# Optimization experiments

Measured on AMD Instinct MI355X. Metric: run time of the kernel, lower is better.

## Reference

```python
import jax, jax.numpy as jnp
import numpy as np
import math

T, R, H, DK = 3, 4, 8, 32   # num_types, num_relations, n_heads, d_k
OUT = H * DK                # out_dim = 256
IN = 256                    # in_dim (== out_dim, required by residual)
B, N = 4, 1024              # batch, max_nodes
LN_EPS = 1e-5


def setup_inputs() -> dict:
    key = jax.random.key(0)
    ks = jax.random.split(key, 12)
    a = math.sqrt(6.0 / (2 * DK))  # xavier_uniform bound for [d_k,d_k]
    w = 0.02
    return {
        "node_features":   jax.random.normal(ks[0], (B, N, IN), jnp.float32),
        "node_types_soft": jax.random.uniform(ks[1], (B, N, T), jnp.float32),
        "adj_matrix_soft": jax.random.uniform(ks[2], (B, N, N), jnp.float32),
        "edge_types_soft": jax.random.uniform(ks[3], (B, N, N, R), jnp.float32),
        "Wq": jax.random.normal(ks[4], (T, IN, OUT), jnp.float32) * w,
        "bq": jnp.zeros((T, OUT), jnp.float32),
        "Wk": jax.random.normal(ks[5], (T, IN, OUT), jnp.float32) * w,
        "bk": jnp.zeros((T, OUT), jnp.float32),
        "Wv": jax.random.normal(ks[6], (T, IN, OUT), jnp.float32) * w,
        "bv": jnp.zeros((T, OUT), jnp.float32),
        "Wa": jax.random.normal(ks[7], (T, OUT, OUT), jnp.float32) * w,
        "ba": jnp.zeros((T, OUT), jnp.float32),
        "rel_pri": jnp.ones((R, H), jnp.float32),
        "rel_att": jax.random.uniform(ks[8], (R, H, DK, DK), jnp.float32, -a, a),
        "rel_msg": jax.random.uniform(ks[9], (R, H, DK, DK), jnp.float32, -a, a),
        "skip": jnp.ones((T,), jnp.float32),
        "ln_gamma": jnp.ones((T, OUT), jnp.float32),
        "ln_beta": jnp.zeros((T, OUT), jnp.float32),
    }


def _single(x, types, adj, erel, Wq, bq, Wk, bk, Wv, bv, Wa, ba,
            rel_pri, rel_att, rel_msg, skip, ln_gamma, ln_beta):
    # x:[N,in], types:[N,T], adj:[N,N], erel:[N,N,R]
    n = x.shape[0]
    sqrt_dk = float(np.sqrt(DK))
    # per-type projections -> [T,N,H,DK]
    Qt = (jnp.einsum('nd,tdo->tno', x, Wq) + bq[:, None, :]).reshape(T, n, H, DK)
    Kt = (jnp.einsum('nd,tdo->tno', x, Wk) + bk[:, None, :]).reshape(T, n, H, DK)
    Vt = (jnp.einsum('nd,tdo->tno', x, Wv) + bv[:, None, :]).reshape(T, n, H, DK)
    # relation-transformed K/V: [T,R,N,H,DK]
    Ksr = jnp.einsum('tnhd,rhde->trnhe', Kt, rel_att)
    Vsr = jnp.einsum('tnhd,rhde->trnhe', Vt, rel_msg)
    # soft-type mixtures (sums over target/source types factor out of the mask)
    Qbar = jnp.einsum('nt,tnhd->nhd', types, Qt)            # target mix
    Kbar = jnp.einsum('nt,trnhd->rnhd', types, Ksr)         # source mix, per relation
    # accumulated (masked, unnormalized) attention logits [N,N,H]
    res_att = jnp.zeros((n, n, H), x.dtype)
    for r in range(R):
        coef = (adj * erel[:, :, r])[:, :, None] * (rel_pri[r] / sqrt_dk)  # [N,N,H]
        res_att = res_att + coef * jnp.einsum('ihd,jhd->ijh', Qbar, Kbar[r])
    # per-target-row softmax over sources (dim j), zeroed if row-sum tiny
    row_sum = res_att.sum(axis=(1, 2))                       # [N]
    attn = jnp.where((row_sum > 1e-6)[:, None, None],
                     jax.nn.softmax(res_att, axis=1), 0.0)
    # aggregated = sum_{s,r,j} attn * masked score * V_{s,r}  (never builds [N,N,H,DK])
    agg = jnp.zeros((n, H, DK), x.dtype)
    for r in range(R):
        coef = (adj * erel[:, :, r])[:, :, None] * (rel_pri[r] / sqrt_dk)
        for s in range(T):
            score = coef * types[None, :, s, None] * jnp.einsum('ihd,jhd->ijh', Qbar, Ksr[s, r])
            agg = agg + jnp.einsum('ijh,ijh,jhd->ihd', attn, score, Vsr[s, r])
    agg = agg.reshape(n, OUT)
    # per-type output head: a_linear(gelu(agg)), gated residual, layernorm, soft-type mix
    g = jax.nn.gelu(agg, approximate=False)
    trans = jnp.einsum('no,tod->tnd', g, Wa) + ba[:, None, :]          # [T,N,OUT]
    alpha = jax.nn.sigmoid(skip)[:, None, None]
    res = trans * alpha + x[None] * (1.0 - alpha)
    mu = res.mean(axis=-1, keepdims=True)
    var = ((res - mu) ** 2).mean(axis=-1, keepdims=True)
    ln = (res - mu) / jnp.sqrt(var + LN_EPS) * ln_gamma[:, None, :] + ln_beta[:, None, :]
    return jnp.einsum('nt,tnd->nd', types, ln)


def reference(node_features, node_types_soft, adj_matrix_soft, edge_types_soft,
              Wq, bq, Wk, bk, Wv, bv, Wa, ba, rel_pri, rel_att, rel_msg,
              skip, ln_gamma, ln_beta):
    f = jax.vmap(_single, in_axes=(0, 0, 0, 0) + (None,) * 14)
    return f(node_features, node_types_soft, adj_matrix_soft, edge_types_soft,
             Wq, bq, Wk, bk, Wv, bv, Wa, ba, rel_pri, rel_att, rel_msg,
             skip, ln_gamma, ln_beta)
```

## Files before the change

kernel.cpp:

```cpp
#include <hip/hip_runtime.h>
#include <math.h>

constexpr int CB = 4, CN = 1024, CT = 3, CR = 4, CH = 8, CDK = 32, COUT = 256;

typedef __attribute__((ext_vector_type(4))) float f32x4;
typedef __attribute__((ext_vector_type(8))) short s16x8;
typedef __attribute__((ext_vector_type(4))) _Float16 f16x4;
typedef __attribute__((ext_vector_type(8))) _Float16 f16x8;
typedef __attribute__((ext_vector_type(4))) unsigned short u16x4;
typedef __attribute__((ext_vector_type(8))) unsigned short u16x8;

__device__ inline unsigned short f2bf(float x) {
    unsigned u = __float_as_uint(x);
    unsigned r = (u + 0x7fffu + ((u >> 16) & 1u)) >> 16;
    return (unsigned short)r;
}
__device__ inline float bf2f(unsigned short b) {
    return __uint_as_float(((unsigned)b) << 16);
}

__global__ void zero_rs(float* __restrict__ rs) {
    rs[blockIdx.x * 256 + threadIdx.x] = 0.f;
}

__global__ __launch_bounds__(256) void gemm_kernel(
    int mode,
    const float* __restrict__ X,
    const float* __restrict__ W0, const float* __restrict__ W1, const float* __restrict__ W2,
    const float* __restrict__ b0, const float* __restrict__ b1, const float* __restrict__ b2,
    float* __restrict__ Y0, float* __restrict__ Y1, float* __restrict__ Y2)
{
    int z = blockIdx.z;
    int b, t, w3;
    if (mode == 0) { b = z / 9; int r9 = z % 9; w3 = r9 / 3; t = r9 % 3; }
    else           { b = z / CT; t = z % CT; w3 = 0; }
    const float* Xb = X + (size_t)b * CN * COUT;
    const float* W  = (w3 == 0 ? W0 : (w3 == 1 ? W1 : W2)) + (size_t)t * COUT * COUT;
    const float* bs = (w3 == 0 ? b0 : (w3 == 1 ? b1 : b2)) + t * COUT;
    float* Y = (w3 == 0 ? Y0 : (w3 == 1 ? Y1 : Y2)) + ((size_t)b * CT + t) * CN * COUT;

    int row0 = blockIdx.x * 64, col0 = blockIdx.y * 64;
    __shared__ float As[16][65];
    __shared__ float Bsh[16][64];
    int tid = threadIdx.x;
    int tx = tid & 15, ty = tid >> 4;
    float acc[4][4] = {};

    for (int kt = 0; kt < COUT; kt += 16) {
        {
            int m = tid >> 2, k4 = (tid & 3) * 4;
            float4 xv = *(const float4*)(Xb + (size_t)(row0 + m) * COUT + kt + k4);
            As[k4 + 0][m] = xv.x; As[k4 + 1][m] = xv.y;
            As[k4 + 2][m] = xv.z; As[k4 + 3][m] = xv.w;
            int kk = tid >> 4, n4 = (tid & 15) * 4;
            *(float4*)(&Bsh[kk][n4]) = *(const float4*)(W + (size_t)(kt + kk) * COUT + col0 + n4);
        }
        __syncthreads();
        #pragma unroll
        for (int kk = 0; kk < 16; ++kk) {
            float a0 = As[kk][ty * 4 + 0], a1 = As[kk][ty * 4 + 1];
            float a2 = As[kk][ty * 4 + 2], a3 = As[kk][ty * 4 + 3];
            float4 bv = *(const float4*)(&Bsh[kk][tx * 4]);
            acc[0][0] += a0 * bv.x; acc[0][1] += a0 * bv.y; acc[0][2] += a0 * bv.z; acc[0][3] += a0 * bv.w;
            acc[1][0] += a1 * bv.x; acc[1][1] += a1 * bv.y; acc[1][2] += a1 * bv.z; acc[1][3] += a1 * bv.w;
            acc[2][0] += a2 * bv.x; acc[2][1] += a2 * bv.y; acc[2][2] += a2 * bv.z; acc[2][3] += a2 * bv.w;
            acc[3][0] += a3 * bv.x; acc[3][1] += a3 * bv.y; acc[3][2] += a3 * bv.z; acc[3][3] += a3 * bv.w;
        }
        __syncthreads();
    }
    float4 bb = *(const float4*)(bs + col0 + tx * 4);
    #pragma unroll
    for (int im = 0; im < 4; ++im) {
        float4 o;
        o.x = acc[im][0] + bb.x; o.y = acc[im][1] + bb.y;
        o.z = acc[im][2] + bb.z; o.w = acc[im][3] + bb.w;
        *(float4*)(Y + (size_t)(row0 + ty * 4 + im) * COUT + col0 + tx * 4) = o;
    }
}

__global__ void mix_qbar(const float* __restrict__ Qt, const float* __restrict__ types,
                         float* __restrict__ Qbar)
{
    int idx = blockIdx.x * 256 + threadIdx.x;
    int bi = idx >> 6;
    int o4 = (idx & 63) * 4;
    int b = bi >> 10;
    const float* tp = types + (size_t)bi * CT;
    float t0 = tp[0], t1 = tp[1], t2 = tp[2];
    size_t nbase = ((size_t)b * CT) * CN * COUT + (size_t)(bi & 1023) * COUT + o4;
    float4 q0 = *(const float4*)(Qt + nbase);
    float4 q1 = *(const float4*)(Qt + nbase + (size_t)CN * COUT);
    float4 q2 = *(const float4*)(Qt + nbase + 2 * (size_t)CN * COUT);
    float4 o;
    o.x = t0 * q0.x + t1 * q1.x + t2 * q2.x;
    o.y = t0 * q0.y + t1 * q1.y + t2 * q2.y;
    o.z = t0 * q0.z + t1 * q1.z + t2 * q2.z;
    o.w = t0 * q0.w + t1 * q1.w + t2 * q2.w;
    *(float4*)(Qbar + (size_t)bi * COUT + o4) = o;
}

__global__ __launch_bounds__(256) void qr3_kernel(const float* __restrict__ Qbar,
                                                  const float* __restrict__ rel_att,
                                                  const float* __restrict__ rel_pri,
                                                  unsigned short* __restrict__ Qrhi,
                                                  unsigned short* __restrict__ Qrlo)
{
    int i0 = blockIdx.x * 8;
    int rh = blockIdx.y; int r = rh >> 3, h = rh & 7;
    int b = blockIdx.z;
    __shared__ float A_s[32][33];
    __shared__ float q_s[8][32];
    int tid = threadIdx.x;
    {
        int f = tid * 4; int d = f >> 5, e = f & 31;
        float4 v = *(const float4*)(rel_att + ((size_t)rh * 32 + d) * 32 + e);
        A_s[d][e] = v.x; A_s[d][e + 1] = v.y; A_s[d][e + 2] = v.z; A_s[d][e + 3] = v.w;
        int ii = tid >> 5, ee = tid & 31;
        q_s[ii][ee] = Qbar[((size_t)b * CN + i0 + ii) * COUT + h * CDK + ee];
    }
    __syncthreads();
    int d = tid & 31, ii = tid >> 5;
    float acc = 0.f;
    #pragma unroll 8
    for (int e = 0; e < 32; ++e) acc += A_s[d][e] * q_s[ii][e];
    const float inv_sqrt = 0.17677669529663687f;
    float v = acc * rel_pri[rh] * inv_sqrt;
    unsigned short hb = f2bf(v);
    float lo = v - bf2f(hb);
    size_t oidx = ((((size_t)b * CR + r) * CH + h) * CN + i0 + ii) * CDK + d;
    Qrhi[oidx] = hb;
    Qrlo[oidx] = f2bf(lo);
}

__global__ __launch_bounds__(256) void prep_k(const float* __restrict__ Kt,
                                              const float* __restrict__ types,
                                              unsigned short* __restrict__ Kbh,
                                              unsigned short* __restrict__ Kbl,
                                              unsigned short* __restrict__ Kty)
{
    int b = blockIdx.y;
    int j = blockIdx.x * 8 + (threadIdx.x >> 5);
    int c = threadIdx.x & 31;
    int h = c >> 2, d0 = (c & 3) * 8;
    const float* tp = types + ((size_t)b * CN + j) * CT;
    float kb[8];
    #pragma unroll
    for (int k = 0; k < 8; ++k) kb[k] = 0.f;
    #pragma unroll
    for (int s = 0; s < 3; ++s) {
        float ty = tp[s];
        const float* src = Kt + (((size_t)(b * 3 + s)) * CN + j) * COUT + c * 8;
        f32x4 a0 = *(const f32x4*)(src);
        f32x4 a1 = *(const f32x4*)(src + 4);
        u16x8 kt8;
        #pragma unroll
        for (int k = 0; k < 4; ++k) {
            float v0 = ty * a0[k], v1 = ty * a1[k];
            kt8[k] = f2bf(v0); kt8[4 + k] = f2bf(v1);
            kb[k] += v0; kb[4 + k] += v1;
        }
        *(u16x8*)(Kty + (((size_t)(b * 3 + s) * CH + h) * CN + j) * CDK + d0) = kt8;
    }
    u16x8 hv, lv;
    #pragma unroll
    for (int k = 0; k < 8; ++k) {
        unsigned short hb = f2bf(kb[k]);
        hv[k] = hb; lv[k] = f2bf(kb[k] - bf2f(hb));
    }
    *(u16x8*)(Kbh + (((size_t)b * CH + h) * CN + j) * CDK + d0) = hv;
    *(u16x8*)(Kbl + (((size_t)b * CH + h) * CN + j) * CDK + d0) = lv;
}

__global__ __launch_bounds__(256) void vT_kernel(const float* __restrict__ Vt,
                                                 _Float16* __restrict__ VT)
{
    int j0 = blockIdx.x * 64; int h = blockIdx.y; int bs = blockIdx.z;
    __shared__ float tile[32][72];
    int t = threadIdx.x;
    int jj = t >> 2, e8 = (t & 3) * 8;
    const float* src = Vt + ((size_t)bs * CN + j0 + jj) * COUT + h * CDK + e8;
    f32x4 v0 = *(const f32x4*)(src);
    f32x4 v1 = *(const f32x4*)(src + 4);
    #pragma unroll
    for (int k = 0; k < 4; ++k) { tile[e8 + k][jj] = v0[k]; tile[e8 + 4 + k][jj] = v1[k]; }
    __syncthreads();
    int e = t >> 3, jr = (t & 7) * 8;
    f16x8 o;
    #pragma unroll
    for (int k = 0; k < 8; ++k) o[k] = (_Float16)tile[e][jr + k];
    *(f16x8*)(VT + (((size_t)bs * CH + h) * CDK + e) * CN + j0 + jr) = o;
}

__global__ void mT_kernel(const float* __restrict__ rel_msg, _Float16* __restrict__ MT)
{
    int rh = blockIdx.x; int t = threadIdx.x;
    int e = t >> 3, ep4 = (t & 7) * 4;
    f16x4 o;
    #pragma unroll
    for (int k = 0; k < 4; ++k)
        o[k] = (_Float16)rel_msg[((size_t)rh * 32 + ep4 + k) * 32 + e];
    *(f16x4*)(MT + ((size_t)rh * 32 + e) * 32 + ep4) = o;
}

__global__ __launch_bounds__(256) void coef_t(const float* __restrict__ adj,
                                              const float* __restrict__ erel,
                                              float* __restrict__ coefT)
{
    int b = blockIdx.z; int i0 = blockIdx.y * 32; int j0 = blockIdx.x * 32;
    __shared__ float tile[32][132];
    int t = threadIdx.x;
    {
        int ii = t >> 3, jc = t & 7;
        size_t arow = ((size_t)b * CN + i0 + ii) * CN + j0;
        f32x4 av = *(const f32x4*)(adj + arow + jc * 4);
        #pragma unroll
        for (int kk = 0; kk < 4; ++kk) {
            int j = jc * 4 + kk;
            f32x4 ev = *(const f32x4*)(erel + (arow + j) * 4);
            float a = av[kk];
            f32x4 cv;
            cv[0] = ev[0] * a; cv[1] = ev[1] * a; cv[2] = ev[2] * a; cv[3] = ev[3] * a;
            *(f32x4*)&tile[j][ii * 4] = cv;
        }
    }
    __syncthreads();
    {
        int jj = t >> 3, ic = t & 7;
        size_t orow = ((size_t)b * CN + j0 + jj) * CN + i0;
        #pragma unroll
        for (int kk = 0; kk < 4; ++kk)
            *(f32x4*)(coefT + (orow + ic * 4 + kk) * 4) = *(const f32x4*)&tile[jj][(ic * 4 + kk) * 4];
    }
}

__global__ __launch_bounds__(256, 3) void attn3_kernel(
    const unsigned short* __restrict__ Qrhi, const unsigned short* __restrict__ Qrlo,
    const unsigned short* __restrict__ Kbh,  const unsigned short* __restrict__ Kbl,
    const unsigned short* __restrict__ Kty,
    const _Float16* __restrict__ VT,
    const float* __restrict__ coefT,
    float* __restrict__ Upart,
    float* __restrict__ lbuf,
    float* __restrict__ rowsum)
{
    const int h = blockIdx.y;
    const int z = blockIdx.z; const int b = z >> 1, part = z & 1;
    const int tid = threadIdx.x;
    const int wave = tid >> 6, lane = tid & 63;
    const int col = lane & 15, quad = lane >> 4;
    const int i = blockIdx.x * 64 + wave * 16 + col;
    const int jbase = part * 512;

    __shared__ _Float16 vs[2][3][32][20];

    s16x8 qh[4], ql[4];
    #pragma unroll
    for (int r = 0; r < 4; ++r) {
        size_t off = ((((size_t)b * CR + r) * CH + h) * CN + i) * CDK + quad * 8;
        qh[r] = *(const s16x8*)(Qrhi + off);
        ql[r] = *(const s16x8*)(Qrlo + off);
    }

    const int e_st = tid >> 3, jc_st = tid & 7;
    size_t vtb[3];
    #pragma unroll
    for (int s = 0; s < 3; ++s)
        vtb[s] = (((size_t)(b * 3 + s) * CH + h) * CDK + e_st) * CN + jc_st * 2;

    #pragma unroll
    for (int s = 0; s < 3; ++s)
        *(unsigned*)&vs[0][s][e_st][jc_st * 2] = *(const unsigned*)(VT + vtb[s] + jbase);
    __syncthreads();

    f32x4 U[4][2];
    #pragma unroll
    for (int r = 0; r < 4; ++r) { U[r][0] = (f32x4){0.f,0.f,0.f,0.f}; U[r][1] = (f32x4){0.f,0.f,0.f,0.f}; }
    float lpart = 0.f, rspart = 0.f;

    const size_t kbbase = (((size_t)b * CH + h) * CN + col) * CDK + quad * 8;
    size_t ktbase[3];
    #pragma unroll
    for (int s = 0; s < 3; ++s)
        ktbase[s] = (((size_t)(b * 3 + s) * CH + h) * CN + col) * CDK + quad * 8;

    #pragma unroll 1
    for (int js = 0; js < 32; ++js) {
        const int j0 = jbase + js * 16;
        const int buf = js & 1;
        const int jn = jbase + ((js + 1 < 32) ? (js + 1) * 16 : js * 16);
        unsigned pf0 = *(const unsigned*)(VT + vtb[0] + jn);
        unsigned pf1 = *(const unsigned*)(VT + vtb[1] + jn);
        unsigned pf2 = *(const unsigned*)(VT + vtb[2] + jn);

        s16x8 kbh_ = *(const s16x8*)(Kbh + kbbase + (size_t)j0 * CDK);
        s16x8 kbl_ = *(const s16x8*)(Kbl + kbbase + (size_t)j0 * CDK);
        s16x8 kt[3];
        #pragma unroll
        for (int s = 0; s < 3; ++s)
            kt[s] = *(const s16x8*)(Kty + ktbase[s] + (size_t)j0 * CDK);
        f32x4 cf[4];
        #pragma unroll
        for (int reg = 0; reg < 4; ++reg)
            cf[reg] = *(const f32x4*)(coefT + (((size_t)b * CN + j0 + quad * 4 + reg) * CN + i) * 4);

        f32x4 Db[4];
        #pragma unroll
        for (int r = 0; r < 4; ++r) {
            f32x4 d = {0.f, 0.f, 0.f, 0.f};
            d = __builtin_amdgcn_mfma_f32_16x16x32_bf16(kbl_, qh[r], d, 0, 0, 0);
            d = __builtin_amdgcn_mfma_f32_16x16x32_bf16(kbh_, ql[r], d, 0, 0, 0);
            d = __builtin_amdgcn_mfma_f32_16x16x32_bf16(kbh_, qh[r], d, 0, 0, 0);
            Db[r] = d;
        }
        float P[4];
        #pragma unroll
        for (int reg = 0; reg < 4; ++reg) {
            float L = cf[reg][0] * Db[0][reg] + cf[reg][1] * Db[1][reg]
                    + cf[reg][2] * Db[2][reg] + cf[reg][3] * Db[3][reg];
            rspart += L;
            P[reg] = __expf(L);
            lpart += P[reg];
        }
        #pragma unroll
        for (int s = 0; s < 3; ++s) {
            f32x4 Dp[4];
            #pragma unroll
            for (int r = 0; r < 4; ++r) {
                f32x4 d = {0.f, 0.f, 0.f, 0.f};
                Dp[r] = __builtin_amdgcn_mfma_f32_16x16x32_bf16(kt[s], qh[r], d, 0, 0, 0);
            }
            f16x4 v0 = *(const f16x4*)&vs[buf][s][col][quad * 4];
            f16x4 v1 = *(const f16x4*)&vs[buf][s][col + 16][quad * 4];
            #pragma unroll
            for (int r = 0; r < 4; ++r) {
                f16x4 w;
                w[0] = (_Float16)(P[0] * cf[0][r] * Dp[r][0]);
                w[1] = (_Float16)(P[1] * cf[1][r] * Dp[r][1]);
                w[2] = (_Float16)(P[2] * cf[2][r] * Dp[r][2]);
                w[3] = (_Float16)(P[3] * cf[3][r] * Dp[r][3]);
                U[r][0] = __builtin_amdgcn_mfma_f32_16x16x16f16(v0, w, U[r][0], 0, 0, 0);
                U[r][1] = __builtin_amdgcn_mfma_f32_16x16x16f16(v1, w, U[r][1], 0, 0, 0);
            }
        }
        *(unsigned*)&vs[buf ^ 1][0][e_st][jc_st * 2] = pf0;
        *(unsigned*)&vs[buf ^ 1][1][e_st][jc_st * 2] = pf1;
        *(unsigned*)&vs[buf ^ 1][2][e_st][jc_st * 2] = pf2;
        __syncthreads();
    }

    float l = lpart;  l += __shfl_xor(l, 16);  l += __shfl_xor(l, 32);
    float rv = rspart; rv += __shfl_xor(rv, 16); rv += __shfl_xor(rv, 32);
    if (quad == 0) {
        lbuf[(((size_t)part * CB + b) * CH + h) * CN + i] = l;
        atomicAdd(rowsum + (size_t)b * CN + i, rv);
    }
    int itile = blockIdx.x * 4 + wave;
    size_t ub = ((((size_t)(b * CH + h) * 64 + itile) * 2 + part)) * 2048;
    #pragma unroll
    for (int r = 0; r < 4; ++r)
        #pragma unroll
        for (int eh = 0; eh < 2; ++eh)
            *(f32x4*)(Upart + ub + (size_t)(r * 2 + eh) * 256 + lane * 4) = U[r][eh];
}

__global__ __launch_bounds__(256) void merge_kernel(
    const float* __restrict__ Upart, const float* __restrict__ lbuf,
    const _Float16* __restrict__ MT, float* __restrict__ agg)
{
    const int h = blockIdx.y, b = blockIdx.z;
    const int tid = threadIdx.x;
    const int wave = tid >> 6, lane = tid & 63;
    const int col = lane & 15, quad = lane >> 4;
    const int itile = blockIdx.x * 4 + wave;
    const int i = itile * 16 + col;

    size_t ub = ((size_t)(b * CH + h) * 64 + itile) * 2 * 2048;
    f32x4 U[4][2];
    #pragma unroll
    for (int r = 0; r < 4; ++r)
        #pragma unroll
        for (int eh = 0; eh < 2; ++eh) {
            f32x4 a = *(const f32x4*)(Upart + ub + (size_t)(r * 2 + eh) * 256 + lane * 4);
            f32x4 c = *(const f32x4*)(Upart + ub + 2048 + (size_t)(r * 2 + eh) * 256 + lane * 4);
            U[r][eh] = a + c;
        }
    float l = lbuf[(((size_t)0 * CB + b) * CH + h) * CN + i]
            + lbuf[(((size_t)1 * CB + b) * CH + h) * CN + i];
    float il = 1.f / l;
    f16x4 Uh[4][2];
    #pragma unroll
    for (int r = 0; r < 4; ++r)
        #pragma unroll
        for (int eh = 0; eh < 2; ++eh) {
            Uh[r][eh][0] = (_Float16)(U[r][eh][0] * il);
            Uh[r][eh][1] = (_Float16)(U[r][eh][1] * il);
            Uh[r][eh][2] = (_Float16)(U[r][eh][2] * il);
            Uh[r][eh][3] = (_Float16)(U[r][eh][3] * il);
        }
    #pragma unroll
    for (int eo = 0; eo < 2; ++eo) {
        f32x4 acc = {0.f, 0.f, 0.f, 0.f};
        #pragma unroll
        for (int r = 0; r < 4; ++r)
            #pragma unroll
            for (int ep = 0; ep < 2; ++ep) {
                f16x4 mt = *(const f16x4*)(MT + ((size_t)(r * 8 + h) * 32 + eo * 16 + col) * 32
                                               + ep * 16 + quad * 4);
                acc = __builtin_amdgcn_mfma_f32_16x16x16f16(mt, Uh[r][ep], acc, 0, 0, 0);
            }
        *(f32x4*)(agg + ((size_t)b * CN + i) * COUT + h * CDK + eo * 16 + quad * 4) = acc;
    }
}

__global__ void gelu_gate(const float* __restrict__ agg, const float* __restrict__ row_sum,
                          float* __restrict__ gout)
{
    int idx = blockIdx.x * 256 + threadIdx.x;
    int bi = idx >> 6;
    float rsv = row_sum[bi];
    float4 v = *(const float4*)(agg + (size_t)idx * 4);
    if (!(rsv > 1e-6f)) { v.x = 0.f; v.y = 0.f; v.z = 0.f; v.w = 0.f; }
    const float is2 = 0.70710678118654752f;
    float4 o;
    o.x = 0.5f * v.x * (1.f + erff(v.x * is2));
    o.y = 0.5f * v.y * (1.f + erff(v.y * is2));
    o.z = 0.5f * v.z * (1.f + erff(v.z * is2));
    o.w = 0.5f * v.w * (1.f + erff(v.w * is2));
    *(float4*)(gout + (size_t)idx * 4) = o;
}

__global__ __launch_bounds__(256) void final_ln(
    const float* __restrict__ trans, const float* __restrict__ x,
    const float* __restrict__ types, const float* __restrict__ skip,
    const float* __restrict__ gamma, const float* __restrict__ beta,
    float* __restrict__ out)
{
    int bi = blockIdx.x;
    int b = bi >> 10;
    int i = bi & 1023;
    int o = threadIdx.x;
    __shared__ float red[4];
    float xo = x[(size_t)bi * COUT + o];
    float accum = 0.f;
    #pragma unroll 1
    for (int t = 0; t < CT; ++t) {
        float al = 1.f / (1.f + __expf(-skip[t]));
        float tr = trans[(((size_t)b * CT + t) * CN + i) * COUT + o];
        float res = tr * al + xo * (1.f - al);
        float v = res;
        #pragma unroll
        for (int mk = 1; mk < 64; mk <<= 1) v += __shfl_xor(v, mk);
        __syncthreads();
        if ((o & 63) == 0) red[o >> 6] = v;
        __syncthreads();
        float mu = (red[0] + red[1] + red[2] + red[3]) * (1.f / COUT);
        float dc = res - mu;
        float v2 = dc * dc;
        #pragma unroll
        for (int mk = 1; mk < 64; mk <<= 1) v2 += __shfl_xor(v2, mk);
        __syncthreads();
        if ((o & 63) == 0) red[o >> 6] = v2;
        __syncthreads();
        float var = (red[0] + red[1] + red[2] + red[3]) * (1.f / COUT);
        float ln = dc * rsqrtf(var + 1e-5f) * gamma[t * COUT + o] + beta[t * COUT + o];
        accum += types[(size_t)bi * CT + t] * ln;
    }
    out[(size_t)bi * COUT + o] = accum;
}

extern "C" void kernel_launch(void* const* d_in, const int* in_sizes, int n_in,
                              void* d_out, int out_size, void* d_ws, size_t ws_size,
                              hipStream_t stream)
{
    (void)in_sizes; (void)n_in; (void)out_size; (void)ws_size;
    const float* nf      = (const float*)d_in[0];
    const float* types   = (const float*)d_in[1];
    const float* adj     = (const float*)d_in[2];
    const float* erel    = (const float*)d_in[3];
    const float* Wq      = (const float*)d_in[4];
    const float* bq      = (const float*)d_in[5];
    const float* Wk      = (const float*)d_in[6];
    const float* bk      = (const float*)d_in[7];
    const float* Wv      = (const float*)d_in[8];
    const float* bv      = (const float*)d_in[9];
    const float* Wa      = (const float*)d_in[10];
    const float* ba      = (const float*)d_in[11];
    const float* rel_pri = (const float*)d_in[12];
    const float* rel_att = (const float*)d_in[13];
    const float* rel_msg = (const float*)d_in[14];
    const float* skip    = (const float*)d_in[15];
    const float* gamma   = (const float*)d_in[16];
    const float* beta    = (const float*)d_in[17];
    float* out = (float*)d_out;

    float* ws = (float*)d_ws;
    size_t o = 0;
    float* pool0 = ws + o; o += 3 * (size_t)CB * CT * CN * COUT;
    float* Qt  = pool0;
    float* Ktb = pool0 + (size_t)CB * CT * CN * COUT;
    float* Vtb = pool0 + 2 * (size_t)CB * CT * CN * COUT;
    float* Qbar = ws + o; o += (size_t)CB * CN * COUT;
    float* aggb = ws + o; o += (size_t)CB * CN * COUT;
    float* rsb  = ws + o; o += (size_t)CB * CN;
    float* lbufp = ws + o; o += 2 * (size_t)CB * CH * CN;
    unsigned short* Qrhi = (unsigned short*)(ws + o); o += (size_t)CB * CR * CN * COUT / 2;
    unsigned short* Qrlo = (unsigned short*)(ws + o); o += (size_t)CB * CR * CN * COUT / 2;
    unsigned short* Kbh  = (unsigned short*)(ws + o); o += (size_t)CB * CH * CN * CDK / 2;
    unsigned short* Kbl  = (unsigned short*)(ws + o); o += (size_t)CB * CH * CN * CDK / 2;
    unsigned short* Kty  = (unsigned short*)(ws + o); o += (size_t)CB * CT * CH * CN * CDK / 2;
    _Float16* VTb = (_Float16*)(ws + o);              o += (size_t)CB * CT * CH * CDK * CN / 2;
    _Float16* MTb = (_Float16*)(ws + o);              o += (size_t)CR * CH * CDK * CDK / 2;
    float* coefT = ws + o; o += (size_t)CB * CN * CN * CR;
    float* Upart  = pool0;
    float* gbuf   = pool0;
    float* transb = pool0 + (size_t)CB * CN * COUT;

    zero_rs<<<CB * CN / 256, 256, 0, stream>>>(rsb);
    gemm_kernel<<<dim3(16, 4, CB * 9), 256, 0, stream>>>(0, nf, Wq, Wk, Wv, bq, bk, bv, Qt, Ktb, Vtb);
    coef_t<<<dim3(32, 32, CB), 256, 0, stream>>>(adj, erel, coefT);
    mix_qbar<<<CB * CN * COUT / 4 / 256, 256, 0, stream>>>(Qt, types, Qbar);
    qr3_kernel<<<dim3(CN / 8, CR * CH, CB), 256, 0, stream>>>(Qbar, rel_att, rel_pri, Qrhi, Qrlo);
    prep_k<<<dim3(CN / 8, CB), 256, 0, stream>>>(Ktb, types, Kbh, Kbl, Kty);
    vT_kernel<<<dim3(CN / 64, CH, CB * CT), 256, 0, stream>>>(Vtb, VTb);
    mT_kernel<<<CR * CH, 256, 0, stream>>>(rel_msg, MTb);
    attn3_kernel<<<dim3(16, CH, CB * 2), 256, 0, stream>>>(Qrhi, Qrlo, Kbh, Kbl, Kty, VTb, coefT,
                                                           Upart, lbufp, rsb);
    merge_kernel<<<dim3(16, CH, CB), 256, 0, stream>>>(Upart, lbufp, MTb, aggb);
    gelu_gate<<<CB * CN * COUT / 4 / 256, 256, 0, stream>>>(aggb, rsb, gbuf);
    gemm_kernel<<<dim3(16, 4, CB * CT), 256, 0, stream>>>(1, gbuf, Wa, Wa, Wa, ba, ba, ba,
                                                          transb, transb, transb);
    final_ln<<<CB * CN, 256, 0, stream>>>(transb, nf, types, skip, gamma, beta, out);
}
```

Baseline: 440.3 us.

## Move projection and output GEMMs to split-bf16 MFMA, fuse GELU into merge

Replaces the FP32 SIMT tiled GEMMs for the Q/K/V and output projections with a bf16 MFMA GEMM. Accuracy is kept by splitting inputs and weights into hi/lo bf16 pairs and using three MFMA products. GELU and the row-sum gate are folded into the merge kernel, which writes split-bf16 activations directly, so the separate gelu pass and the agg buffer go away. Layernorm now handles one row per wave with vectorised loads and no block syncs. The cost is extra split and transpose kernels and a small loss of precision from dropping the lo*lo term.

```diff
diff --git a/kernel.cpp b/kernel.cpp
--- a/kernel.cpp
+++ b/kernel.cpp
@@ -23,59 +23,144 @@
     rs[blockIdx.x * 256 + threadIdx.x] = 0.f;
 }
 
-__global__ __launch_bounds__(256) void gemm_kernel(
+__global__ void splitx(const float* __restrict__ X,
+                       unsigned short* __restrict__ Xh, unsigned short* __restrict__ Xl)
+{
+    size_t idx = ((size_t)blockIdx.x * 256 + threadIdx.x) * 4;
+    f32x4 v = *(const f32x4*)(X + idx);
+    u16x4 hv, lv;
+    #pragma unroll
+    for (int k = 0; k < 4; ++k) {
+        unsigned short hb = f2bf(v[k]);
+        hv[k] = hb;
+        lv[k] = f2bf(v[k] - bf2f(hb));
+    }
+    *(u16x4*)(Xh + idx) = hv;
+    *(u16x4*)(Xl + idx) = lv;
+}
+
+__global__ __launch_bounds__(256) void wsplit(
+    const float* __restrict__ Wq, const float* __restrict__ Wk,
+    const float* __restrict__ Wv, const float* __restrict__ Wa,
+    unsigned short* __restrict__ WTh, unsigned short* __restrict__ WTl)
+{
+    int z = blockIdx.z;
+    int t = z % 3;
+    const float* W;
+    if (z < 9) { int w3 = z / 3; W = (w3 == 0 ? Wq : (w3 == 1 ? Wk : Wv)); }
+    else W = Wa;
+    W += (size_t)t * COUT * COUT;
+    int k0 = blockIdx.x * 32, n0 = blockIdx.y * 32;
+    __shared__ float tl[32][33];
+    int tid = threadIdx.x;
+    {
+        int k = tid >> 3, n4 = (tid & 7) * 4;
+        f32x4 v = *(const f32x4*)(W + (size_t)(k0 + k) * COUT + n0 + n4);
+        tl[n4 + 0][k] = v[0]; tl[n4 + 1][k] = v[1];
+        tl[n4 + 2][k] = v[2]; tl[n4 + 3][k] = v[3];
+    }
+    __syncthreads();
+    int n = tid >> 3, k4 = (tid & 7) * 4;
+    u16x4 hv, lv;
+    #pragma unroll
+    for (int j = 0; j < 4; ++j) {
+        float x = tl[n][k4 + j];
+        unsigned short hb = f2bf(x);
+        hv[j] = hb; lv[j] = f2bf(x - bf2f(hb));
+    }
+    size_t off = (size_t)z * COUT * COUT + (size_t)(n0 + n) * COUT + k0 + k4;
+    *(u16x4*)(WTh + off) = hv;
+    *(u16x4*)(WTl + off) = lv;
+}
+
+__global__ __launch_bounds__(256) void mfma_gemm(
     int mode,
-    const float* __restrict__ X,
-    const float* __restrict__ W0, const float* __restrict__ W1, const float* __restrict__ W2,
-    const float* __restrict__ b0, const float* __restrict__ b1, const float* __restrict__ b2,
+    const unsigned short* __restrict__ Ah, const unsigned short* __restrict__ Al,
+    const unsigned short* __restrict__ WTh, const unsigned short* __restrict__ WTl,
+    const float* __restrict__ bq, const float* __restrict__ bk,
+    const float* __restrict__ bv, const float* __restrict__ ba,
     float* __restrict__ Y0, float* __restrict__ Y1, float* __restrict__ Y2)
 {
     int z = blockIdx.z;
-    int b, t, w3;
-    if (mode == 0) { b = z / 9; int r9 = z % 9; w3 = r9 / 3; t = r9 % 3; }
-    else           { b = z / CT; t = z % CT; w3 = 0; }
-    const float* Xb = X + (size_t)b * CN * COUT;
-    const float* W  = (w3 == 0 ? W0 : (w3 == 1 ? W1 : W2)) + (size_t)t * COUT * COUT;
-    const float* bs = (w3 == 0 ? b0 : (w3 == 1 ? b1 : b2)) + t * COUT;
-    float* Y = (w3 == 0 ? Y0 : (w3 == 1 ? Y1 : Y2)) + ((size_t)b * CT + t) * CN * COUT;
-
-    int row0 = blockIdx.x * 64, col0 = blockIdx.y * 64;
-    __shared__ float As[16][65];
-    __shared__ float Bsh[16][64];
-    int tid = threadIdx.x;
-    int tx = tid & 15, ty = tid >> 4;
-    float acc[4][4] = {};
-
-    for (int kt = 0; kt < COUT; kt += 16) {
-        {
-            int m = tid >> 2, k4 = (tid & 3) * 4;
-            float4 xv = *(const float4*)(Xb + (size_t)(row0 + m) * COUT + kt + k4);
-            As[k4 + 0][m] = xv.x; As[k4 + 1][m] = xv.y;
-            As[k4 + 2][m] = xv.z; As[k4 + 3][m] = xv.w;
-            int kk = tid >> 4, n4 = (tid & 15) * 4;
-            *(float4*)(&Bsh[kk][n4]) = *(const float4*)(W + (size_t)(kt + kk) * COUT + col0 + n4);
+    int b, t, widx;
+    const float* bias;
+    float* Y;
+    if (mode == 0) {
+        b = z / 9; int r9 = z % 9; int w3 = r9 / 3; t = r9 % 3;
+        widx = w3 * 3 + t;
+        bias = (w3 == 0 ? bq : (w3 == 1 ? bk : bv)) + t * COUT;
+        Y = (w3 == 0 ? Y0 : (w3 == 1 ? Y1 : Y2)) + ((size_t)b * CT + t) * CN * COUT;
+    } else {
+        b = z / CT; t = z % CT;
+        widx = 9 + t;
+        bias = ba + t * COUT;
+        Y = Y0 + ((size_t)b * CT + t) * CN * COUT;
+    }
+    const unsigned short* Ahb = Ah + (size_t)b * CN * COUT;
+    const unsigned short* Alb = Al + (size_t)b * CN * COUT;
+    const unsigned short* Bhb = WTh + (size_t)widx * COUT * COUT;
+    const unsigned short* Blb = WTl + (size_t)widx * COUT * COUT;
+
+    const int M0 = blockIdx.x * 128, N0 = blockIdx.y * 128;
+    __shared__ unsigned short As[2][128][40];
+    __shared__ unsigned short Bs[2][128][40];
+    const int tid = threadIdx.x;
+    const int wave = tid >> 6, lane = tid & 63;
+    const int wm = wave & 1, wn = wave >> 1;
+    const int col = lane & 15, quad = lane >> 4;
+
+    f32x4 acc[4][4];
+    #pragma unroll
+    for (int mt = 0; mt < 4; ++mt)
+        #pragma unroll
+        for (int nt = 0; nt < 4; ++nt) acc[mt][nt] = (f32x4){0.f, 0.f, 0.f, 0.f};
+
+    for (int kt = 0; kt < COUT; kt += 32) {
+        #pragma unroll
+        for (int q = 0; q < 2; ++q) {
+            int f = q * 256 + tid;
+            int m = f >> 2, kc = (f & 3) * 8;
+            *(u16x8*)&As[0][m][kc] = *(const u16x8*)(Ahb + (size_t)(M0 + m) * COUT + kt + kc);
+            *(u16x8*)&As[1][m][kc] = *(const u16x8*)(Alb + (size_t)(M0 + m) * COUT + kt + kc);
+            *(u16x8*)&Bs[0][m][kc] = *(const u16x8*)(Bhb + (size_t)(N0 + m) * COUT + kt + kc);
+            *(u16x8*)&Bs[1][m][kc] = *(const u16x8*)(Blb + (size_t)(N0 + m) * COUT + kt + kc);
         }
         __syncthreads();
-        #pragma unroll
-        for (int kk = 0; kk < 16; ++kk) {
-            float a0 = As[kk][ty * 4 + 0], a1 = As[kk][ty * 4 + 1];
-            float a2 = As[kk][ty * 4 + 2], a3 = As[kk][ty * 4 + 3];
-            float4 bv = *(const float4*)(&Bsh[kk][tx * 4]);
-            acc[0][0] += a0 * bv.x; acc[0][1] += a0 * bv.y; acc[0][2] += a0 * bv.z; acc[0][3] += a0 * bv.w;
-            acc[1][0] += a1 * bv.x; acc[1][1] += a1 * bv.y; acc[1][2] += a1 * bv.z; acc[1][3] += a1 * bv.w;
-            acc[2][0] += a2 * bv.x; acc[2][1] += a2 * bv.y; acc[2][2] += a2 * bv.z; acc[2][3] += a2 * bv.w;
-            acc[3][0] += a3 * bv.x; acc[3][1] += a3 * bv.y; acc[3][2] += a3 * bv.z; acc[3][3] += a3 * bv.w;
-        }
+        s16x8 ah[4], al4[4], bh[4], bl4[4];
+        #pragma unroll
+        for (int mt = 0; mt < 4; ++mt) {
+            ah[mt]  = *(const s16x8*)&As[0][wm * 64 + mt * 16 + col][quad * 8];
+            al4[mt] = *(const s16x8*)&As[1][wm * 64 + mt * 16 + col][quad * 8];
+        }
+        #pragma unroll
+        for (int nt = 0; nt < 4; ++nt) {
+            bh[nt]  = *(const s16x8*)&Bs[0][wn * 64 + nt * 16 + col][quad * 8];
+            bl4[nt] = *(const s16x8*)&Bs[1][wn * 64 + nt * 16 + col][quad * 8];
+        }
+        #pragma unroll
+        for (int mt = 0; mt < 4; ++mt)
+            #pragma unroll
+            for (int nt = 0; nt < 4; ++nt) {
+                acc[mt][nt] = __builtin_amdgcn_mfma_f32_16x16x32_bf16(al4[mt], bh[nt], acc[mt][nt], 0, 0, 0);
+                acc[mt][nt] = __builtin_amdgcn_mfma_f32_16x16x32_bf16(ah[mt], bl4[nt], acc[mt][nt], 0, 0, 0);
+                acc[mt][nt] = __builtin_amdgcn_mfma_f32_16x16x32_bf16(ah[mt], bh[nt], acc[mt][nt], 0, 0, 0);
+            }
         __syncthreads();
     }
-    float4 bb = *(const float4*)(bs + col0 + tx * 4);
-    #pragma unroll
-    for (int im = 0; im < 4; ++im) {
-        float4 o;
-        o.x = acc[im][0] + bb.x; o.y = acc[im][1] + bb.y;
-        o.z = acc[im][2] + bb.z; o.w = acc[im][3] + bb.w;
-        *(float4*)(Y + (size_t)(row0 + ty * 4 + im) * COUT + col0 + tx * 4) = o;
-    }
+    float bb[4];
+    #pragma unroll
+    for (int nt = 0; nt < 4; ++nt) bb[nt] = bias[N0 + wn * 64 + nt * 16 + col];
+    #pragma unroll
+    for (int mt = 0; mt < 4; ++mt)
+        #pragma unroll
+        for (int nt = 0; nt < 4; ++nt) {
+            int n = N0 + wn * 64 + nt * 16 + col;
+            #pragma unroll
+            for (int reg = 0; reg < 4; ++reg) {
+                int m = M0 + wm * 64 + mt * 16 + quad * 4 + reg;
+                Y[(size_t)m * COUT + n] = acc[mt][nt][reg] + bb[nt];
+            }
+        }
 }
 
 __global__ void mix_qbar(const float* __restrict__ Qt, const float* __restrict__ types,
@@ -363,9 +448,10 @@
             *(f32x4*)(Upart + ub + (size_t)(r * 2 + eh) * 256 + lane * 4) = U[r][eh];
 }
 
-__global__ __launch_bounds__(256) void merge_kernel(
+__global__ __launch_bounds__(256) void merge_gelu(
     const float* __restrict__ Upart, const float* __restrict__ lbuf,
-    const _Float16* __restrict__ MT, float* __restrict__ agg)
+    const _Float16* __restrict__ MT, const float* __restrict__ rowsum,
+    unsigned short* __restrict__ Gh, unsigned short* __restrict__ Gl)
 {
     const int h = blockIdx.y, b = blockIdx.z;
     const int tid = threadIdx.x;
@@ -397,6 +483,9 @@
             Uh[r][eh][2] = (_Float16)(U[r][eh][2] * il);
             Uh[r][eh][3] = (_Float16)(U[r][eh][3] * il);
         }
+    float rsv = rowsum[(size_t)b * CN + i];
+    bool gate = rsv > 1e-6f;
+    const float is2 = 0.70710678118654752f;
     #pragma unroll
     for (int eo = 0; eo < 2; ++eo) {
         f32x4 acc = {0.f, 0.f, 0.f, 0.f};
@@ -408,64 +497,56 @@
                                                + ep * 16 + quad * 4);
                 acc = __builtin_amdgcn_mfma_f32_16x16x16f16(mt, Uh[r][ep], acc, 0, 0, 0);
             }
-        *(f32x4*)(agg + ((size_t)b * CN + i) * COUT + h * CDK + eo * 16 + quad * 4) = acc;
-    }
-}
-
-__global__ void gelu_gate(const float* __restrict__ agg, const float* __restrict__ row_sum,
-                          float* __restrict__ gout)
-{
-    int idx = blockIdx.x * 256 + threadIdx.x;
-    int bi = idx >> 6;
-    float rsv = row_sum[bi];
-    float4 v = *(const float4*)(agg + (size_t)idx * 4);
-    if (!(rsv > 1e-6f)) { v.x = 0.f; v.y = 0.f; v.z = 0.f; v.w = 0.f; }
-    const float is2 = 0.70710678118654752f;
-    float4 o;
-    o.x = 0.5f * v.x * (1.f + erff(v.x * is2));
-    o.y = 0.5f * v.y * (1.f + erff(v.y * is2));
-    o.z = 0.5f * v.z * (1.f + erff(v.z * is2));
-    o.w = 0.5f * v.w * (1.f + erff(v.w * is2));
-    *(float4*)(gout + (size_t)idx * 4) = o;
-}
-
-__global__ __launch_bounds__(256) void final_ln(
+        u16x4 hv, lv;
+        #pragma unroll
+        for (int k = 0; k < 4; ++k) {
+            float x = gate ? acc[k] : 0.f;
+            float g = 0.5f * x * (1.f + erff(x * is2));
+            unsigned short hb = f2bf(g);
+            hv[k] = hb; lv[k] = f2bf(g - bf2f(hb));
+        }
+        size_t off = ((size_t)b * CN + i) * COUT + h * CDK + eo * 16 + quad * 4;
+        *(u16x4*)(Gh + off) = hv;
+        *(u16x4*)(Gl + off) = lv;
+    }
+}
+
+__global__ __launch_bounds__(256) void final_ln2(
     const float* __restrict__ trans, const float* __restrict__ x,
     const float* __restrict__ types, const float* __restrict__ skip,
     const float* __restrict__ gamma, const float* __restrict__ beta,
     float* __restrict__ out)
 {
-    int bi = blockIdx.x;
-    int b = bi >> 10;
-    int i = bi & 1023;
-    int o = threadIdx.x;
-    __shared__ float red[4];
-    float xo = x[(size_t)bi * COUT + o];
-    float accum = 0.f;
+    int wave = threadIdx.x >> 6, lane = threadIdx.x & 63;
+    int bi = blockIdx.x * 4 + wave;
+    int b = bi >> 10, i = bi & 1023;
+    f32x4 xo = *(const f32x4*)(x + (size_t)bi * COUT + lane * 4);
+    f32x4 accum = {0.f, 0.f, 0.f, 0.f};
+    const float* tp = types + (size_t)bi * CT;
     #pragma unroll 1
     for (int t = 0; t < CT; ++t) {
         float al = 1.f / (1.f + __expf(-skip[t]));
-        float tr = trans[(((size_t)b * CT + t) * CN + i) * COUT + o];
-        float res = tr * al + xo * (1.f - al);
-        float v = res;
-        #pragma unroll
-        for (int mk = 1; mk < 64; mk <<= 1) v += __shfl_xor(v, mk);
-        __syncthreads();
-        if ((o & 63) == 0) red[o >> 6] = v;
-        __syncthreads();
-        float mu = (red[0] + red[1] + red[2] + red[3]) * (1.f / COUT);
-        float dc = res - mu;
-        float v2 = dc * dc;
-        #pragma unroll
-        for (int mk = 1; mk < 64; mk <<= 1) v2 += __shfl_xor(v2, mk);
-        __syncthreads();
-        if ((o & 63) == 0) red[o >> 6] = v2;
-        __syncthreads();
-        float var = (red[0] + red[1] + red[2] + red[3]) * (1.f / COUT);
-        float ln = dc * rsqrtf(var + 1e-5f) * gamma[t * COUT + o] + beta[t * COUT + o];
-        accum += types[(size_t)bi * CT + t] * ln;
-    }
-    out[(size_t)bi * COUT + o] = accum;
+        f32x4 tr = *(const f32x4*)(trans + (((size_t)b * CT + t) * CN + i) * COUT + lane * 4);
+        f32x4 res;
+        float s = 0.f;
+        #pragma unroll
+        for (int k = 0; k < 4; ++k) { res[k] = tr[k] * al + xo[k] * (1.f - al); s += res[k]; }
+        #pragma unroll
+        for (int mk = 1; mk < 64; mk <<= 1) s += __shfl_xor(s, mk);
+        float mu = s * (1.f / COUT);
+        f32x4 dc; float s2 = 0.f;
+        #pragma unroll
+        for (int k = 0; k < 4; ++k) { dc[k] = res[k] - mu; s2 += dc[k] * dc[k]; }
+        #pragma unroll
+        for (int mk = 1; mk < 64; mk <<= 1) s2 += __shfl_xor(s2, mk);
+        float inv = rsqrtf(s2 * (1.f / COUT) + 1e-5f);
+        f32x4 g = *(const f32x4*)(gamma + (size_t)t * COUT + lane * 4);
+        f32x4 be = *(const f32x4*)(beta + (size_t)t * COUT + lane * 4);
+        float ty = tp[t];
+        #pragma unroll
+        for (int k = 0; k < 4; ++k) accum[k] += ty * (dc[k] * inv * g[k] + be[k]);
+    }
+    *(f32x4*)(out + (size_t)bi * COUT + lane * 4) = accum;
 }
 
 extern "C" void kernel_launch(void* const* d_in, const int* in_sizes, int n_in,
@@ -500,7 +581,6 @@
     float* Ktb = pool0 + (size_t)CB * CT * CN * COUT;
     float* Vtb = pool0 + 2 * (size_t)CB * CT * CN * COUT;
     float* Qbar = ws + o; o += (size_t)CB * CN * COUT;
-    float* aggb = ws + o; o += (size_t)CB * CN * COUT;
     float* rsb  = ws + o; o += (size_t)CB * CN;
     float* lbufp = ws + o; o += 2 * (size_t)CB * CH * CN;
     unsigned short* Qrhi = (unsigned short*)(ws + o); o += (size_t)CB * CR * CN * COUT / 2;
@@ -510,13 +590,21 @@
     unsigned short* Kty  = (unsigned short*)(ws + o); o += (size_t)CB * CT * CH * CN * CDK / 2;
     _Float16* VTb = (_Float16*)(ws + o);              o += (size_t)CB * CT * CH * CDK * CN / 2;
     _Float16* MTb = (_Float16*)(ws + o);              o += (size_t)CR * CH * CDK * CDK / 2;
+    unsigned short* Xh = (unsigned short*)(ws + o);   o += (size_t)CB * CN * COUT / 2;
+    unsigned short* Xl = (unsigned short*)(ws + o);   o += (size_t)CB * CN * COUT / 2;
+    unsigned short* Gh = (unsigned short*)(ws + o);   o += (size_t)CB * CN * COUT / 2;
+    unsigned short* Gl = (unsigned short*)(ws + o);   o += (size_t)CB * CN * COUT / 2;
+    unsigned short* WTh = (unsigned short*)(ws + o);  o += (size_t)12 * COUT * COUT / 2;
+    unsigned short* WTl = (unsigned short*)(ws + o);  o += (size_t)12 * COUT * COUT / 2;
     float* coefT = ws + o; o += (size_t)CB * CN * CN * CR;
     float* Upart  = pool0;
-    float* gbuf   = pool0;
-    float* transb = pool0 + (size_t)CB * CN * COUT;
+    float* transb = pool0 + 3 * (size_t)CB * CN * COUT;
 
     zero_rs<<<CB * CN / 256, 256, 0, stream>>>(rsb);
-    gemm_kernel<<<dim3(16, 4, CB * 9), 256, 0, stream>>>(0, nf, Wq, Wk, Wv, bq, bk, bv, Qt, Ktb, Vtb);
+    splitx<<<CB * CN * COUT / 4 / 256, 256, 0, stream>>>(nf, Xh, Xl);
+    wsplit<<<dim3(8, 8, 12), 256, 0, stream>>>(Wq, Wk, Wv, Wa, WTh, WTl);
+    mfma_gemm<<<dim3(8, 2, CB * 9), 256, 0, stream>>>(0, Xh, Xl, WTh, WTl,
+                                                      bq, bk, bv, ba, Qt, Ktb, Vtb);
     coef_t<<<dim3(32, 32, CB), 256, 0, stream>>>(adj, erel, coefT);
     mix_qbar<<<CB * CN * COUT / 4 / 256, 256, 0, stream>>>(Qt, types, Qbar);
     qr3_kernel<<<dim3(CN / 8, CR * CH, CB), 256, 0, stream>>>(Qbar, rel_att, rel_pri, Qrhi, Qrlo);
@@ -525,9 +613,8 @@
     mT_kernel<<<CR * CH, 256, 0, stream>>>(rel_msg, MTb);
     attn3_kernel<<<dim3(16, CH, CB * 2), 256, 0, stream>>>(Qrhi, Qrlo, Kbh, Kbl, Kty, VTb, coefT,
                                                            Upart, lbufp, rsb);
-    merge_kernel<<<dim3(16, CH, CB), 256, 0, stream>>>(Upart, lbufp, MTb, aggb);
-    gelu_gate<<<CB * CN * COUT / 4 / 256, 256, 0, stream>>>(aggb, rsb, gbuf);
-    gemm_kernel<<<dim3(16, 4, CB * CT), 256, 0, stream>>>(1, gbuf, Wa, Wa, Wa, ba, ba, ba,
-                                                          transb, transb, transb);
-    final_ln<<<CB * CN, 256, 0, stream>>>(transb, nf, types, skip, gamma, beta, out);
-}
+    merge_gelu<<<dim3(16, CH, CB), 256, 0, stream>>>(Upart, lbufp, MTb, rsb, Gh, Gl);
+    mfma_gemm<<<dim3(8, 2, CB * CT), 256, 0, stream>>>(1, Gh, Gl, WTh, WTl,
+                                                       bq, bk, bv, ba, transb, transb, transb);
+    final_ln2<<<CB * CN / 4, 256, 0, stream>>>(transb, nf, types, skip, gamma, beta, out);
+}
```

After: 383.1 us. 1.15x faster.
